# Performance work log

Hardware: AMD Instinct MI355X
Metric: run time of the kernel (lower is better)

## Reference

```python
import jax, jax.numpy as jnp
import numpy as np

B, T, N, F_FEAT = 2, 1024, 263, 2
D = 263                # d_model
C = N * F_FEAT         # 526 = d_model * n_features
WINDOW = 25
K_T = int(T * 0.1)     # temporal masked steps
K_F = int(T * 0.1)     # masked frequency bins (<= T//2+1)


def positional_encoding(t, d):
    pos = jnp.arange(t, dtype=jnp.float32)[:, None]
    div = jnp.exp(jnp.arange(0, d, 2, dtype=jnp.float32) * (-np.log(10000.0) / d))
    pe = jnp.zeros((t, d), dtype=jnp.float32)
    pe = pe.at[:, 0::2].set(jnp.sin(pos * div))
    n_odd = pe[:, 1::2].shape[1]
    pe = pe.at[:, 1::2].set(jnp.cos(pos * div[:n_odd]))
    return pe


def setup_inputs() -> dict:
    key = jax.random.key(0)
    ks = jax.random.split(key, 10)
    s = 0.02
    return {
        "x": jax.random.normal(ks[0], (B, T, N, F_FEAT), dtype=jnp.float32),
        "W_emb": jax.random.normal(ks[1], (D, C), dtype=jnp.float32) * s,
        "b_emb": jnp.zeros((D,), jnp.float32),
        "t_token": jax.random.normal(ks[2], (D,), dtype=jnp.float32) * s,
        "W1t": jax.random.normal(ks[3], (D, D), dtype=jnp.float32) * s,
        "b1t": jnp.zeros((D,), jnp.float32),
        "W2t": jax.random.normal(ks[4], (D, D), dtype=jnp.float32) * s,
        "b2t": jnp.zeros((D,), jnp.float32),
        "f_token_r": jax.random.normal(ks[5], (D,), dtype=jnp.float32) * s,
        "f_token_i": jax.random.normal(ks[6], (D,), dtype=jnp.float32) * s,
        "w1f": jax.random.normal(ks[7], (D,), dtype=jnp.float32) * s,
        "b1f": jnp.zeros((D,), jnp.float32),
        "w2f": jax.random.normal(ks[8], (D,), dtype=jnp.float32) * s,
        "b2f": jnp.zeros((1,), jnp.float32),
    }


def _forward(x, W_emb, b_emb, t_token, W1t, b1t, W2t, b2t,
             f_token_r, f_token_i, w1f, b1f, w2f, b2f):
    pe = positional_encoding(T, D)
    # DataEmbedding (dropout inactive / eval) + positional embedding
    ex = x.reshape(B, T, C) @ W_emb.T + b_emb + pe            # [B,T,D]
    bidx = jnp.arange(B)[:, None]

    # ---- temporal masking: causal sliding mean/var (== conv1d ones kernel) ----
    counts = jnp.minimum(jnp.arange(T, dtype=jnp.float32) + 1.0, float(WINDOW))[None, :, None]

    def causal_mean(v):
        cs = jnp.cumsum(v, axis=1)
        shifted = jnp.concatenate([jnp.zeros((B, WINDOW, D), v.dtype), cs[:, :-WINDOW]], axis=1)
        return (cs - shifted) / counts

    m1 = causal_mean(ex)
    var = causal_mean(ex * ex) - m1 * m1
    score = var.sum(-1) / (m1.sum(-1) + 1e-6)                 # [B,T]
    _, idx_t = jax.lax.top_k(score, K_T)                      # [B,K_T]
    masked = ex.at[bidx, idx_t].set(t_token)
    mask_t = jnp.zeros((B, T), bool).at[bidx, idx_t].set(True)
    h = jax.nn.gelu(masked @ W1t.T + b1t, approximate=False)
    proj = jax.nn.sigmoid(h @ W2t.T + b2t)
    masked = jnp.where(mask_t[..., None], masked, proj)
    out_t = (masked @ W_emb).reshape(B, T, N, F_FEAT)         # weight.T @ x^T, transposed

    # ---- frequency masking ----
    cx = jnp.fft.rfft(ex, axis=1)                             # [B, T//2+1, D]
    mag = jnp.abs(cx)
    _, idx_f = jax.lax.top_k(mag.mean(axis=2), K_F)           # [B,K_F]
    token_c = (f_token_r + 1j * f_token_i).astype(cx.dtype)
    cxm = cx.at[bidx, idx_f].set(token_c)
    xt = jnp.fft.irfft(cxm, n=T, axis=1)                      # [B,T,D]
    fm = jnp.zeros((B, T // 2 + 1), jnp.float32).at[bidx, idx_f].set(1.0)
    mask_f = jnp.fft.irfft(fm, n=T, axis=1) != 0              # [B,T] (same for all channels)
    v = xt @ W_emb                                            # [B,T,C]
    # per-scalar MLP: Linear(1,D)+GELU+Linear(D,1)+Sigmoid
    hf = jax.nn.gelu(v[..., None] * w1f + b1f, approximate=False)   # [B,T,C,D]
    projf = jax.nn.sigmoid(jnp.einsum('btcd,d->btc', hf, w2f) + b2f)
    out_f = jnp.where(mask_f[:, :, None], v, projf).reshape(B, T, N, F_FEAT)

    return out_t, idx_t, out_f, idx_f


def reference(x, W_emb, b_emb, t_token, W1t, b1t, W2t, b2t,
              f_token_r, f_token_i, w1f, b1f, w2f, b2f):
    return _forward(x, W_emb, b_emb, t_token, W1t, b1t, W2t, b2t,
                    f_token_r, f_token_i, w1f, b1f, w2f, b2f)
```

## Files before the change

kernel.cpp:

```cpp
#include <hip/hip_runtime.h>

#define TDIM 1024
#define DD   263
#define CC   526
#define NFREQ 513
#define PACK 1026
#define KTOP 102

static const size_t WS_EX     = 0;
static const size_t WS_W1BF   = 538624;
static const size_t WS_W2BF   = 584704;
static const size_t WS_WEMT   = 630784;
static const size_t WS_MASKB  = 1615872;
static const size_t WS_XTBF   = 1910784;
static const size_t WS_HBF    = 2693120;
static const size_t WS_CXP    = 3770368;
static const size_t WS_EXTHL  = 4310044;
static const size_t WS_ITSEL  = 5360668;
static const size_t WS_DELTA  = 5901340;
static const size_t WS_TABC   = 6411292;
static const size_t WS_TABS   = 6412316;
static const size_t WS_SCORE  = 6413340;
static const size_t WS_MAGM   = 6417436;
static const size_t WS_MASKT  = 6419488;
static const size_t WS_IDXT   = 6421536;
static const size_t WS_IDXF   = 6421740;
static const size_t WS_MASKF  = 6421944;
static const size_t WS_XHL    = 6422972;
static const size_t WS_THL    = 8094140;
static const size_t WS_WHL    = 9765308;
static const size_t WS_TOTAL  = 10740380;

static const size_t OFF_OUTT = 0;
static const size_t OFF_IDXT = 1077248;
static const size_t OFF_OUTF = 1077452;
static const size_t OFF_IDXF = 2154700;

typedef __bf16 bf16x8_t __attribute__((ext_vector_type(8)));
typedef float  f32x4_t  __attribute__((ext_vector_type(4)));

__device__ __forceinline__ unsigned short f2bf(float f) {
    unsigned int u = __float_as_uint(f);
    unsigned int r = (u + 0x7fffu + ((u >> 16) & 1u)) >> 16;
    return (unsigned short)r;
}
__device__ __forceinline__ float bf2f(unsigned short h) {
    return __uint_as_float(((unsigned int)h) << 16);
}

__device__ __forceinline__ float pe_val(int t, int d) {
    const float sc = (float)(-9.210340371976184 / 263.0);
    int j = d >> 1;
    float div = expf((float)(2 * j) * sc);
    float a = (float)t * div;
    return (d & 1) ? cosf(a) : sinf(a);
}

#define WG_FENCE()   asm volatile("" ::: "memory")
#define WG_BARRIER() { WG_FENCE(); __builtin_amdgcn_s_barrier(); WG_FENCE(); }
#define WAVE_LDS_SYNC() { asm volatile("s_waitcnt lgkmcnt(0)" ::: "memory"); __builtin_amdgcn_sched_barrier(0); }

template<int EPI, int KU>
__device__ __forceinline__ void gemm_body(int hw, int nwg,
                                          const unsigned short* __restrict__ A,
                                          const unsigned short* __restrict__ Bt,
                                          const float* __restrict__ bias,
                                          void* __restrict__ Cv,
                                          void* __restrict__ aux,
                                          int M, int N, int SA, int NC, int gy)
{
    __shared__ unsigned short As[64][32 * KU + 8];
    __shared__ unsigned short Bs[64][32 * KU + 8];
    const int q = nwg >> 3, r = nwg & 7, xcd = hw & 7;
    const int logical = (xcd < r ? xcd * (q + 1) : r * (q + 1) + (xcd - r) * q) + (hw >> 3);
    const int row0 = (logical / gy) * 64, col0 = (logical % gy) * 64;
    if (EPI == 7) Bt += (size_t)(row0 >> 10) * 320 * SA;

    const int tid  = threadIdx.x;
    const int wid = tid >> 6, lane = tid & 63;
    const int wr = wid >> 1, wc = wid & 1;
    const int srow = tid >> 2, skoff = (tid & 3) * 8;
    const int fl = lane & 15, fh = lane >> 4;
    f32x4_t acc[2][2];
#pragma unroll
    for (int i = 0; i < 2; i++)
#pragma unroll
        for (int j = 0; j < 2; j++) acc[i][j] = (f32x4_t){0.f, 0.f, 0.f, 0.f};

    const int nk = SA / (32 * KU);
    const unsigned short* pa = A  + (size_t)(row0 + srow) * SA + skoff;
    const unsigned short* pb = Bt + (size_t)(col0 + srow) * SA + skoff;

    bf16x8_t qa[4][KU], qb[4][KU];
#pragma unroll
    for (int j = 0; j < 4; ++j) {
        if (j < nk) {
#pragma unroll
            for (int u = 0; u < KU; ++u) {
                qa[j][u] = *(const bf16x8_t*)(pa + (size_t)j * (32 * KU) + u * 32);
                qb[j][u] = *(const bf16x8_t*)(pb + (size_t)j * (32 * KU) + u * 32);
            }
        }
    }

    for (int itb = 0; itb < nk; itb += 4) {
#pragma unroll
        for (int j = 0; j < 4; ++j) {
            const int it = itb + j;
            if (it < nk) {
                if (it > 0) WG_BARRIER();
#pragma unroll
                for (int u = 0; u < KU; ++u) {
                    *(bf16x8_t*)(&As[srow][u * 32 + skoff]) = qa[j][u];
                    *(bf16x8_t*)(&Bs[srow][u * 32 + skoff]) = qb[j][u];
                }
                asm volatile("s_waitcnt lgkmcnt(0)" ::: "memory");
                WG_BARRIER();
#pragma unroll
                for (int u = 0; u < KU; ++u) {
                    bf16x8_t fa0 = *(const bf16x8_t*)(&As[wr * 32 + fl][u * 32 + fh * 8]);
                    bf16x8_t fa1 = *(const bf16x8_t*)(&As[wr * 32 + 16 + fl][u * 32 + fh * 8]);
                    bf16x8_t fb0 = *(const bf16x8_t*)(&Bs[wc * 32 + fl][u * 32 + fh * 8]);
                    bf16x8_t fb1 = *(const bf16x8_t*)(&Bs[wc * 32 + 16 + fl][u * 32 + fh * 8]);
                    acc[0][0] = __builtin_amdgcn_mfma_f32_16x16x32_bf16(fa0, fb0, acc[0][0], 0, 0, 0);
                    acc[0][1] = __builtin_amdgcn_mfma_f32_16x16x32_bf16(fa0, fb1, acc[0][1], 0, 0, 0);
                    acc[1][0] = __builtin_amdgcn_mfma_f32_16x16x32_bf16(fa1, fb0, acc[1][0], 0, 0, 0);
                    acc[1][1] = __builtin_amdgcn_mfma_f32_16x16x32_bf16(fa1, fb1, acc[1][1], 0, 0, 0);
                }
                if (it + 4 < nk) {
#pragma unroll
                    for (int u = 0; u < KU; ++u) {
                        qa[j][u] = *(const bf16x8_t*)(pa + (size_t)(it + 4) * (32 * KU) + u * 32);
                        qb[j][u] = *(const bf16x8_t*)(pb + (size_t)(it + 4) * (32 * KU) + u * 32);
                    }
                }
            }
        }
    }

#pragma unroll
    for (int fi = 0; fi < 2; fi++)
#pragma unroll
        for (int fj = 0; fj < 2; fj++)
#pragma unroll
            for (int rr = 0; rr < 4; rr++) {
                int m = row0 + wr * 32 + fi * 16 + fh * 4 + rr;
                int n = col0 + wc * 32 + fj * 16 + fl;
                if (m >= M) continue;
                float v = acc[fi][fj][rr];
                if (EPI == 0) {
                    if (n < N) ((float*)Cv)[(size_t)m * NC + n] = v;
                } else if (EPI == 1) {
                    if (n < NC) {
                        float o = 0.0f;
                        if (n < N) { o = v + bias[n]; o = 0.5f * o * (1.0f + erff(o * 0.70710678118654752f)); }
                        ((unsigned short*)Cv)[(size_t)m * NC + n] = f2bf(o);
                    }
                } else if (EPI == 4) {
                    if (n < N) {
                        float o = v + bias[n] + pe_val(m & (TDIM - 1), n);
                        ((float*)Cv)[(size_t)m * NC + n] = o;
                        unsigned short hi = f2bf(o);
                        unsigned short lo = f2bf(o - bf2f(hi));
                        size_t b2 = ((size_t)(m >> 10) * 320 + n) * 3072 + (m & 1023);
                        unsigned short* xh = (unsigned short*)aux;
                        xh[b2] = hi; xh[b2 + 1024] = lo; xh[b2 + 2048] = hi;
                    }
                } else if (EPI == 5) {
                    int b = n / 320, col = n - b * 320;
                    if (col < DD) ((float*)Cv)[((size_t)b * PACK + m) * DD + col] = v;
                } else if (EPI == 7) {
                    if (n < 288) {
                        unsigned short o = 0;
                        if (n < DD) o = f2bf(bias[(size_t)m * DD + n] + v);
                        ((unsigned short*)Cv)[(size_t)m * 288 + n] = o;
                    }
                } else if (EPI == 8) {
                    const int* mt = (const int*)aux;
                    if (n < 288 && !mt[m]) {
                        unsigned short o = 0;
                        if (n < DD) {
                            float s = v + bias[n];
                            o = f2bf(1.0f / (1.0f + expf(-s)));
                        }
                        ((unsigned short*)Cv)[(size_t)m * 288 + n] = o;
                    }
                } else {
                    if (n < CC) {
                        size_t off = (m < 2048) ? (size_t)m * CC + n
                                                : (size_t)OFF_OUTF + (size_t)(m - 2048) * CC + n;
                        ((float*)Cv)[off] = v;
                    }
                }
            }
}

template<int EPI, int KU>
__global__ __launch_bounds__(256) void gemm_k(const unsigned short* __restrict__ A,
                                              const unsigned short* __restrict__ Bt,
                                              const float* __restrict__ bias,
                                              void* __restrict__ Cv, void* __restrict__ aux,
                                              int M, int N, int SA, int NC, int gy)
{
    gemm_body<EPI, KU>(blockIdx.x, gridDim.x, A, Bt, bias, Cv, aux, M, N, SA, NC, gy);
}

__device__ __forceinline__ void score_wave(int ib, const float* __restrict__ ex,
                                           double* __restrict__ score) {
    const int t = ib & (TDIM - 1);
    const int lane = threadIdx.x & 63;
    double ms = 0.0, vs = 0.0;
    if (t >= 24) {
        const float* base = ex + (size_t)(ib - 24) * DD;
        for (int d = lane; d < DD; d += 64) {
            float s1 = 0.0f, s2 = 0.0f;
#pragma unroll
            for (int r = 0; r < 25; r++) {
                float v = base[(size_t)r * DD + d];
                s1 += v;
                s2 += v * v;
            }
            float m1 = s1 * (1.0f / 25.0f);
            float var = s2 * (1.0f / 25.0f) - m1 * m1;
            ms += (double)m1;
            vs += (double)var;
        }
    } else {
        const int nt = t + 1;
        const float cnt = (float)nt;
        const float* base = ex + (size_t)(ib - t) * DD;
        for (int d = lane; d < DD; d += 64) {
            float s1 = 0.0f, s2 = 0.0f;
            for (int r = 0; r < nt; r++) {
                float v = base[(size_t)r * DD + d];
                s1 += v;
                s2 += v * v;
            }
            float m1 = s1 / cnt;
            float var = s2 / cnt - m1 * m1;
            ms += (double)m1;
            vs += (double)var;
        }
    }
#pragma unroll
    for (int off = 32; off; off >>= 1) { ms += __shfl_xor(ms, off); vs += __shfl_xor(vs, off); }
    if (lane == 0) score[ib] = vs / (ms + (double)1e-6f);
}

__device__ __forceinline__ void mag_wave(int ib, const float* __restrict__ cxp,
                                         double* __restrict__ magm) {
    int b = ib / NFREQ, k = ib % NFREQ;
    int lane = threadIdx.x & 63;
    const float* re = cxp + ((size_t)b * PACK + k) * DD;
    const float* im = cxp + ((size_t)b * PACK + NFREQ + k) * DD;
    double acc = 0.0;
    for (int d = lane; d < DD; d += 64) {
        float r = re[d], i = im[d];
        acc += (double)sqrtf(r * r + i * i);
    }
#pragma unroll
    for (int off = 32; off; off >>= 1) acc += __shfl_xor(acc, off);
    if (lane == 0) magm[ib] = acc / (double)DD;
}

__device__ __forceinline__ void topk_body(int b, const double* __restrict__ score,
                                          int n, int kcount,
                                          float* __restrict__ out_f, int* __restrict__ out_i,
                                          int* __restrict__ mask) {
    __shared__ double sv[1024];
    __shared__ int    si[1024];
    const int tid = threadIdx.x;
    const double* s = score + (size_t)b * n;
    for (int i = tid; i < 1024; i += 512) {
        sv[i] = (i < n) ? s[i] : -1.0e300;
        si[i] = i;
    }
    __syncthreads();
    for (int k = 2; k <= 1024; k <<= 1) {
        for (int j = k >> 1; j > 0; j >>= 1) {
            int t = ((tid & ~(j - 1)) << 1) | (tid & (j - 1));
            int l = t | j;
            double v0 = sv[t], v1 = sv[l];
            int i0 = si[t], i1 = si[l];
            bool g = (v0 > v1) || (v0 == v1 && i0 < i1);
            bool wrong = ((t & k) == 0) ? !g : g;
            if (wrong) {
                sv[t] = v1; sv[l] = v0;
                si[t] = i1; si[l] = i0;
            }
            int next_j = (j > 1) ? (j >> 1) : k;
            if (j >= 128 || next_j >= 128) __syncthreads();
            else WAVE_LDS_SYNC();
        }
    }
    __syncthreads();
    for (int t = tid; t < kcount; t += 512) {
        int bi = si[t];
        out_f[(size_t)b * kcount + t] = (float)bi;
        out_i[b * kcount + t] = bi;
        mask[b * n + bi] = 1;
    }
}

__device__ __forceinline__ void build_masked_body(int bt, const float* __restrict__ ex,
                                                  const float* __restrict__ ttok,
                                                  const int* __restrict__ maskt,
                                                  unsigned short* __restrict__ mb) {
    int d = threadIdx.x;
    if (d >= 288) return;
    float v = 0.0f;
    if (d < DD) v = maskt[bt] ? ttok[d] : ex[(size_t)bt * DD + d];
    mb[(size_t)bt * 288 + d] = f2bf(v);
}

__device__ __forceinline__ void sel_delta_body(int blk,
                                               const float* __restrict__ tabc, const float* __restrict__ tabs,
                                               const int* __restrict__ idxf, const float* __restrict__ cxp,
                                               const float* __restrict__ ftr, const float* __restrict__ fti,
                                               unsigned short* __restrict__ itsel,
                                               unsigned short* __restrict__ delta) {
    if (blk < 2048) {
        int b = blk >> 10, t = blk & 1023;
        unsigned short* dst = itsel + (size_t)blk * 224;
        for (int j = threadIdx.x; j < 224; j += 256) {
            float v = 0.0f;
            if (j < KTOP) {
                int k = idxf[b * KTOP + j];
                float w = (k == 0 || k == 512) ? 1.0f : 2.0f;
                v = (w * (1.0f / 1024.0f)) * tabc[(k * t) & 1023];
            } else if (j >= 112 && j < 112 + KTOP) {
                int k = idxf[b * KTOP + j - 112];
                v = (k == 0 || k == 512) ? 0.0f : (-2.0f / 1024.0f) * tabs[(k * t) & 1023];
            }
            dst[j] = f2bf(v);
        }
    } else {
        int idx = blk - 2048;
        int b = idx / 320, d = idx - (idx / 320) * 320;
        unsigned short* dst = delta + (size_t)idx * 224;
        for (int j = threadIdx.x; j < 224; j += 256) {
            float v = 0.0f;
            if (d < DD) {
                if (j < KTOP) {
                    int k = idxf[b * KTOP + j];
                    v = ftr[d] - cxp[((size_t)b * PACK + k) * DD + d];
                } else if (j >= 112 && j < 112 + KTOP) {
                    int k = idxf[b * KTOP + j - 112];
                    v = fti[d] - cxp[((size_t)b * PACK + NFREQ + k) * DD + d];
                }
            }
            dst[j] = f2bf(v);
        }
    }
}

__device__ __forceinline__ void thl_row_body(int row, const float* __restrict__ tabc,
                                             const float* __restrict__ tabs,
                                             unsigned short* __restrict__ thl) {
    unsigned short* dst = thl + (size_t)row * 3072;
    for (int c = threadIdx.x; c < 3072; c += 256) {
        int seg = c >> 10, t = c & 1023;
        float v = 0.0f;
        if (row < PACK) v = (row < NFREQ) ? tabc[(row * t) & 1023] : -tabs[((row - NFREQ) * t) & 1023];
        unsigned short hi = f2bf(v);
        dst[c] = (seg < 2) ? hi : f2bf(v - bf2f(hi));
    }
}

__global__ __launch_bounds__(256) void initconv_k(int* maskt, int* maskf, float* tabc, float* tabs,
                                                  const float* __restrict__ W1t,
                                                  const float* __restrict__ W2t,
                                                  const float* __restrict__ W_emb,
                                                  const float* __restrict__ x,
                                                  unsigned short* __restrict__ w1b,
                                                  unsigned short* __restrict__ w2b,
                                                  unsigned short* __restrict__ wemT,
                                                  unsigned short* __restrict__ xhl,
                                                  unsigned short* __restrict__ whl)
{
    int blk = blockIdx.x;
    if (blk < 8) {
        int i = blk * 256 + threadIdx.x;
        if (i < 2 * TDIM) maskt[i] = 0;
        if (i < PACK) maskf[i] = 0;
        if (i < 1024) {
            double ang = (double)i * (3.14159265358979323846 * 2.0 / 1024.0);
            tabc[i] = (float)cos(ang);
            tabs[i] = (float)sin(ang);
        }
    } else if (blk < 1224) {
        int r = blk - 8;
        if (r < 640) {
            int rr = r & 319;
            const float* src = (r < 320) ? W1t : W2t;
            unsigned short* dst = (r < 320) ? w1b : w2b;
            for (int c = threadIdx.x; c < 288; c += 256) {
                float v = (rr < DD && c < DD) ? src[(size_t)rr * DD + c] : 0.0f;
                dst[(size_t)rr * 288 + c] = f2bf(v);
            }
        } else {
            int rr = r - 640;
            for (int c = threadIdx.x; c < 288; c += 256) {
                float v = (rr < CC && c < DD) ? W_emb[(size_t)c * CC + rr] : 0.0f;
                wemT[(size_t)rr * 288 + c] = f2bf(v);
            }
        }
    } else if (blk < 3272) {
        int r = blk - 1224;
        const float* src = x + (size_t)r * CC;
        unsigned short* dst = xhl + (size_t)r * 1632;
        for (int c = threadIdx.x; c < 1632; c += 256) {
            int seg = c / 544, cc = c - seg * 544;
            float v = (cc < CC) ? src[cc] : 0.0f;
            unsigned short hi = f2bf(v);
            dst[c] = (seg < 2) ? hi : f2bf(v - bf2f(hi));
        }
    } else {
        int n = blk - 3272;
        unsigned short* dst = whl + (size_t)n * 1632;
        for (int c = threadIdx.x; c < 1632; c += 256) {
            int seg = c / 544, cc = c - seg * 544;
            float v = (n < DD && cc < CC) ? W_emb[(size_t)n * CC + cc] : 0.0f;
            unsigned short hi = f2bf(v);
            dst[c] = (seg == 1) ? f2bf(v - bf2f(hi)) : hi;
        }
    }
}

__global__ __launch_bounds__(256) void fused_ex_thl_k(const unsigned short* __restrict__ xhl,
                                                      const unsigned short* __restrict__ whl,
                                                      const float* __restrict__ b_emb,
                                                      float* __restrict__ ex,
                                                      unsigned short* __restrict__ exthl,
                                                      const float* __restrict__ tabc,
                                                      const float* __restrict__ tabs,
                                                      unsigned short* __restrict__ thl)
{
    if (blockIdx.x < 160) {
        gemm_body<4, 3>(blockIdx.x, 160, xhl, whl, b_emb, ex, exthl, 2048, DD, 1632, DD, 5);
    } else {
        thl_row_body(blockIdx.x - 160, tabc, tabs, thl);
    }
}

__global__ __launch_bounds__(256) void fused_dft_score_k(const unsigned short* __restrict__ thl,
                                                         const unsigned short* __restrict__ exthl,
                                                         float* __restrict__ cxp,
                                                         const float* __restrict__ ex,
                                                         double* __restrict__ score)
{
    if (blockIdx.x < 170) {
        gemm_body<5, 4>(blockIdx.x, 170, thl, exthl, nullptr, cxp, nullptr, PACK, 640, 3072, 0, 10);
    } else {
        int ib = (int)(blockIdx.x - 170) * 4 + (threadIdx.x >> 6);
        score_wave(ib, ex, score);
    }
}

__global__ __launch_bounds__(512) void fused_topkt_mag_k(const double* __restrict__ score,
                                                         float* __restrict__ outf, int* __restrict__ idxt,
                                                         int* __restrict__ maskt,
                                                         const float* __restrict__ cxp,
                                                         double* __restrict__ magm)
{
    if (blockIdx.x < 2) {
        topk_body(blockIdx.x, score, TDIM, KTOP, outf, idxt, maskt);
    } else {
        int ib = (int)(blockIdx.x - 2) * 8 + (threadIdx.x >> 6);
        if (ib < 2 * NFREQ) mag_wave(ib, cxp, magm);
    }
}

__global__ __launch_bounds__(512) void fused_topkf_bm_k(const double* __restrict__ magm,
                                                        float* __restrict__ outf, int* __restrict__ idxf,
                                                        int* __restrict__ maskf,
                                                        const float* __restrict__ ex,
                                                        const float* __restrict__ ttok,
                                                        const int* __restrict__ maskt,
                                                        unsigned short* __restrict__ mb)
{
    if (blockIdx.x < 2) {
        topk_body(blockIdx.x, magm, NFREQ, KTOP, outf, idxf, maskf);
    } else {
        build_masked_body(blockIdx.x - 2, ex, ttok, maskt, mb);
    }
}

__global__ __launch_bounds__(256) void fused_h_seldelta_k(const unsigned short* __restrict__ maskb,
                                                          const unsigned short* __restrict__ w1b,
                                                          const float* __restrict__ b1t,
                                                          unsigned short* __restrict__ hb,
                                                          const float* __restrict__ tabc,
                                                          const float* __restrict__ tabs,
                                                          const int* __restrict__ idxf,
                                                          const float* __restrict__ cxp,
                                                          const float* __restrict__ ftr,
                                                          const float* __restrict__ fti,
                                                          unsigned short* __restrict__ itsel,
                                                          unsigned short* __restrict__ delta)
{
    if (blockIdx.x < 160) {
        gemm_body<1, 3>(blockIdx.x, 160, maskb, w1b, b1t, hb, nullptr, 2048, DD, 288, 288, 5);
    } else {
        sel_delta_body(blockIdx.x - 160, tabc, tabs, idxf, cxp, ftr, fti, itsel, delta);
    }
}

__global__ __launch_bounds__(256) void fused_sig_corr_k(const unsigned short* __restrict__ hb,
                                                        const unsigned short* __restrict__ w2b,
                                                        const float* __restrict__ b2t,
                                                        unsigned short* __restrict__ maskb,
                                                        const int* __restrict__ maskt,
                                                        const unsigned short* __restrict__ itsel,
                                                        const unsigned short* __restrict__ delta,
                                                        const float* __restrict__ ex,
                                                        unsigned short* __restrict__ xtb)
{
    if (blockIdx.x < 160) {
        gemm_body<8, 3>(blockIdx.x, 160, hb, w2b, b2t, maskb, (void*)maskt, 2048, DD, 288, 288, 5);
    } else {
        gemm_body<7, 1>(blockIdx.x - 160, 160, itsel, delta, ex, xtb, nullptr, 2048, 320, 224, 288, 5);
    }
}

extern "C" void kernel_launch(void* const* d_in, const int* in_sizes, int n_in,
                              void* d_out, int out_size, void* d_ws, size_t ws_size,
                              hipStream_t stream) {
    (void)in_sizes; (void)n_in; (void)out_size; (void)ws_size;
    const float* x      = (const float*)d_in[0];
    const float* W_emb  = (const float*)d_in[1];
    const float* b_emb  = (const float*)d_in[2];
    const float* ttok   = (const float*)d_in[3];
    const float* W1t    = (const float*)d_in[4];
    const float* b1t    = (const float*)d_in[5];
    const float* W2t    = (const float*)d_in[6];
    const float* b2t    = (const float*)d_in[7];
    const float* ftr    = (const float*)d_in[8];
    const float* fti    = (const float*)d_in[9];
    float* out = (float*)d_out;
    float* ws  = (float*)d_ws;

    float* ex     = ws + WS_EX;
    float* cxp    = ws + WS_CXP;
    float* tabc   = ws + WS_TABC;
    float* tabs   = ws + WS_TABS;
    double* score = (double*)(ws + WS_SCORE);
    double* magm  = (double*)(ws + WS_MAGM);
    int* maskt    = (int*)(ws + WS_MASKT);
    int* idxt     = (int*)(ws + WS_IDXT);
    int* idxf     = (int*)(ws + WS_IDXF);
    int* maskf    = (int*)(ws + WS_MASKF);
    unsigned short* w1b   = (unsigned short*)(ws + WS_W1BF);
    unsigned short* w2b   = (unsigned short*)(ws + WS_W2BF);
    unsigned short* wemT  = (unsigned short*)(ws + WS_WEMT);
    unsigned short* maskb = (unsigned short*)(ws + WS_MASKB);
    unsigned short* hb    = (unsigned short*)(ws + WS_HBF);
    unsigned short* xtb   = (unsigned short*)(ws + WS_XTBF);
    unsigned short* itsel = (unsigned short*)(ws + WS_ITSEL);
    unsigned short* delta = (unsigned short*)(ws + WS_DELTA);
    unsigned short* xhl   = (unsigned short*)(ws + WS_XHL);
    unsigned short* thl   = (unsigned short*)(ws + WS_THL);
    unsigned short* whl   = (unsigned short*)(ws + WS_WHL);
    unsigned short* exthl = (unsigned short*)(ws + WS_EXTHL);

    initconv_k<<<3592, 256, 0, stream>>>(maskt, maskf, tabc, tabs,
                                         W1t, W2t, W_emb, x, w1b, w2b, wemT, xhl, whl);

    fused_ex_thl_k<<<1248, 256, 0, stream>>>(xhl, whl, b_emb, ex, exthl, tabc, tabs, thl);

    fused_dft_score_k<<<682, 256, 0, stream>>>(thl, exthl, cxp, ex, score);

    fused_topkt_mag_k<<<131, 512, 0, stream>>>(score, out + OFF_IDXT, idxt, maskt, cxp, magm);

    fused_topkf_bm_k<<<2050, 512, 0, stream>>>(magm, out + OFF_IDXF, idxf, maskf,
                                               ex, ttok, maskt, maskb);

    fused_h_seldelta_k<<<2848, 256, 0, stream>>>(maskb, w1b, b1t, hb,
                                                 tabc, tabs, idxf, cxp, ftr, fti, itsel, delta);

    fused_sig_corr_k<<<320, 256, 0, stream>>>(hb, w2b, b2t, maskb, maskt,
                                              itsel, delta, ex, xtb);

    gemm_k<9, 3><<<576, 256, 0, stream>>>(maskb, wemT, nullptr, out, nullptr, 4096, CC, 288, CC, 9);
}
```

Baseline: 114.4 us.

## Split DFT GEMM K dimension in two and sum partials in consumers

The DFT GEMM's reduction (length 3072) is split into two halves run by separate workgroups, doubling the number of GEMM blocks from 170 to 340 so more CUs are busy. Each half writes to its own buffer (cxp and a new cxp2), and the consumers (magnitude and sel_delta) add the two partials when reading. This costs an extra output buffer, an extra read in the consumers, and requires the new workspace region not to overlap existing ones.

```diff
diff --git a/kernel.cpp b/kernel.cpp
--- a/kernel.cpp
+++ b/kernel.cpp
@@ -11,6 +11,7 @@
 static const size_t WS_W1BF   = 538624;
 static const size_t WS_W2BF   = 584704;
 static const size_t WS_WEMT   = 630784;
+static const size_t WS_CXP2   = 713728;
 static const size_t WS_MASKB  = 1615872;
 static const size_t WS_XTBF   = 1910784;
 static const size_t WS_HBF    = 2693120;
@@ -67,7 +68,7 @@
                                           const float* __restrict__ bias,
                                           void* __restrict__ Cv,
                                           void* __restrict__ aux,
-                                          int M, int N, int SA, int NC, int gy)
+                                          int M, int N, int SA, int klen, int NC, int gy)
 {
     __shared__ unsigned short As[64][32 * KU + 8];
     __shared__ unsigned short Bs[64][32 * KU + 8];
@@ -87,7 +88,7 @@
 #pragma unroll
         for (int j = 0; j < 2; j++) acc[i][j] = (f32x4_t){0.f, 0.f, 0.f, 0.f};
 
-    const int nk = SA / (32 * KU);
+    const int nk = klen / (32 * KU);
     const unsigned short* pa = A  + (size_t)(row0 + srow) * SA + skoff;
     const unsigned short* pb = Bt + (size_t)(col0 + srow) * SA + skoff;
 
@@ -202,7 +203,7 @@
                                               void* __restrict__ Cv, void* __restrict__ aux,
                                               int M, int N, int SA, int NC, int gy)
 {
-    gemm_body<EPI, KU>(blockIdx.x, gridDim.x, A, Bt, bias, Cv, aux, M, N, SA, NC, gy);
+    gemm_body<EPI, KU>(blockIdx.x, gridDim.x, A, Bt, bias, Cv, aux, M, N, SA, SA, NC, gy);
 }
 
 __device__ __forceinline__ void score_wave(int ib, const float* __restrict__ ex,
@@ -248,14 +249,16 @@
 }
 
 __device__ __forceinline__ void mag_wave(int ib, const float* __restrict__ cxp,
+                                         const float* __restrict__ cxp2,
                                          double* __restrict__ magm) {
     int b = ib / NFREQ, k = ib % NFREQ;
     int lane = threadIdx.x & 63;
-    const float* re = cxp + ((size_t)b * PACK + k) * DD;
-    const float* im = cxp + ((size_t)b * PACK + NFREQ + k) * DD;
+    size_t ro = ((size_t)b * PACK + k) * DD;
+    size_t io = ((size_t)b * PACK + NFREQ + k) * DD;
     double acc = 0.0;
     for (int d = lane; d < DD; d += 64) {
-        float r = re[d], i = im[d];
+        float r = cxp[ro + d] + cxp2[ro + d];
+        float i = cxp[io + d] + cxp2[io + d];
         acc += (double)sqrtf(r * r + i * i);
     }
 #pragma unroll
@@ -315,7 +318,9 @@
 
 __device__ __forceinline__ void sel_delta_body(int blk,
                                                const float* __restrict__ tabc, const float* __restrict__ tabs,
-                                               const int* __restrict__ idxf, const float* __restrict__ cxp,
+                                               const int* __restrict__ idxf,
+                                               const float* __restrict__ cxp,
+                                               const float* __restrict__ cxp2,
                                                const float* __restrict__ ftr, const float* __restrict__ fti,
                                                unsigned short* __restrict__ itsel,
                                                unsigned short* __restrict__ delta) {
@@ -343,10 +348,12 @@
             if (d < DD) {
                 if (j < KTOP) {
                     int k = idxf[b * KTOP + j];
-                    v = ftr[d] - cxp[((size_t)b * PACK + k) * DD + d];
+                    size_t o = ((size_t)b * PACK + k) * DD + d;
+                    v = ftr[d] - (cxp[o] + cxp2[o]);
                 } else if (j >= 112 && j < 112 + KTOP) {
                     int k = idxf[b * KTOP + j - 112];
-                    v = fti[d] - cxp[((size_t)b * PACK + NFREQ + k) * DD + d];
+                    size_t o = ((size_t)b * PACK + NFREQ + k) * DD + d;
+                    v = fti[d] - (cxp[o] + cxp2[o]);
                 }
             }
             dst[j] = f2bf(v);
@@ -437,7 +444,7 @@
                                                       unsigned short* __restrict__ thl)
 {
     if (blockIdx.x < 160) {
-        gemm_body<4, 3>(blockIdx.x, 160, xhl, whl, b_emb, ex, exthl, 2048, DD, 1632, DD, 5);
+        gemm_body<4, 3>(blockIdx.x, 160, xhl, whl, b_emb, ex, exthl, 2048, DD, 1632, 1632, DD, 5);
     } else {
         thl_row_body(blockIdx.x - 160, tabc, tabs, thl);
     }
@@ -446,13 +453,17 @@
 __global__ __launch_bounds__(256) void fused_dft_score_k(const unsigned short* __restrict__ thl,
                                                          const unsigned short* __restrict__ exthl,
                                                          float* __restrict__ cxp,
+                                                         float* __restrict__ cxp2,
                                                          const float* __restrict__ ex,
                                                          double* __restrict__ score)
 {
-    if (blockIdx.x < 170) {
-        gemm_body<5, 4>(blockIdx.x, 170, thl, exthl, nullptr, cxp, nullptr, PACK, 640, 3072, 0, 10);
-    } else {
-        int ib = (int)(blockIdx.x - 170) * 4 + (threadIdx.x >> 6);
+    if (blockIdx.x < 340) {
+        int s = (blockIdx.x >= 170) ? 1 : 0;
+        int hw = blockIdx.x - s * 170;
+        gemm_body<5, 4>(hw, 170, thl + s * 1536, exthl + s * 1536, nullptr,
+                        s ? (void*)cxp2 : (void*)cxp, nullptr, PACK, 640, 3072, 1536, 0, 10);
+    } else {
+        int ib = (int)(blockIdx.x - 340) * 4 + (threadIdx.x >> 6);
         score_wave(ib, ex, score);
     }
 }
@@ -461,13 +472,14 @@
                                                          float* __restrict__ outf, int* __restrict__ idxt,
                                                          int* __restrict__ maskt,
                                                          const float* __restrict__ cxp,
+                                                         const float* __restrict__ cxp2,
                                                          double* __restrict__ magm)
 {
     if (blockIdx.x < 2) {
         topk_body(blockIdx.x, score, TDIM, KTOP, outf, idxt, maskt);
     } else {
         int ib = (int)(blockIdx.x - 2) * 8 + (threadIdx.x >> 6);
-        if (ib < 2 * NFREQ) mag_wave(ib, cxp, magm);
+        if (ib < 2 * NFREQ) mag_wave(ib, cxp, cxp2, magm);
     }
 }
 
@@ -494,15 +506,16 @@
                                                           const float* __restrict__ tabs,
                                                           const int* __restrict__ idxf,
                                                           const float* __restrict__ cxp,
+                                                          const float* __restrict__ cxp2,
                                                           const float* __restrict__ ftr,
                                                           const float* __restrict__ fti,
                                                           unsigned short* __restrict__ itsel,
                                                           unsigned short* __restrict__ delta)
 {
     if (blockIdx.x < 160) {
-        gemm_body<1, 3>(blockIdx.x, 160, maskb, w1b, b1t, hb, nullptr, 2048, DD, 288, 288, 5);
-    } else {
-        sel_delta_body(blockIdx.x - 160, tabc, tabs, idxf, cxp, ftr, fti, itsel, delta);
+        gemm_body<1, 3>(blockIdx.x, 160, maskb, w1b, b1t, hb, nullptr, 2048, DD, 288, 288, 288, 5);
+    } else {
+        sel_delta_body(blockIdx.x - 160, tabc, tabs, idxf, cxp, cxp2, ftr, fti, itsel, delta);
     }
 }
 
@@ -517,9 +530,9 @@
                                                         unsigned short* __restrict__ xtb)
 {
     if (blockIdx.x < 160) {
-        gemm_body<8, 3>(blockIdx.x, 160, hb, w2b, b2t, maskb, (void*)maskt, 2048, DD, 288, 288, 5);
-    } else {
-        gemm_body<7, 1>(blockIdx.x - 160, 160, itsel, delta, ex, xtb, nullptr, 2048, 320, 224, 288, 5);
+        gemm_body<8, 3>(blockIdx.x, 160, hb, w2b, b2t, maskb, (void*)maskt, 2048, DD, 288, 288, 288, 5);
+    } else {
+        gemm_body<7, 1>(blockIdx.x - 160, 160, itsel, delta, ex, xtb, nullptr, 2048, 320, 224, 224, 288, 5);
     }
 }
 
@@ -542,6 +555,7 @@
 
     float* ex     = ws + WS_EX;
     float* cxp    = ws + WS_CXP;
+    float* cxp2   = ws + WS_CXP2;
     float* tabc   = ws + WS_TABC;
     float* tabs   = ws + WS_TABS;
     double* score = (double*)(ws + WS_SCORE);
@@ -568,15 +582,15 @@
 
     fused_ex_thl_k<<<1248, 256, 0, stream>>>(xhl, whl, b_emb, ex, exthl, tabc, tabs, thl);
 
-    fused_dft_score_k<<<682, 256, 0, stream>>>(thl, exthl, cxp, ex, score);
-
-    fused_topkt_mag_k<<<131, 512, 0, stream>>>(score, out + OFF_IDXT, idxt, maskt, cxp, magm);
+    fused_dft_score_k<<<852, 256, 0, stream>>>(thl, exthl, cxp, cxp2, ex, score);
+
+    fused_topkt_mag_k<<<131, 512, 0, stream>>>(score, out + OFF_IDXT, idxt, maskt, cxp, cxp2, magm);
 
     fused_topkf_bm_k<<<2050, 512, 0, stream>>>(magm, out + OFF_IDXF, idxf, maskf,
                                                ex, ttok, maskt, maskb);
 
     fused_h_seldelta_k<<<2848, 256, 0, stream>>>(maskb, w1b, b1t, hb,
-                                                 tabc, tabs, idxf, cxp, ftr, fti, itsel, delta);
+                                                 tabc, tabs, idxf, cxp, cxp2, ftr, fti, itsel, delta);
 
     fused_sig_corr_k<<<320, 256, 0, stream>>>(hb, w2b, b2t, maskb, maskt,
                                               itsel, delta, ex, xtb);
```

Measured after the change: 121.0 us. 1.06x slower.
